# Kernel tuning notes

Measured on AMD Instinct MI355X. Metric: run time of the kernel, lower is better.

## Reference

```python
import jax, jax.numpy as jnp
import numpy as np

LATENT_DIM = 128
KQ_DIM = 32
B, N, K = 8, 16384, 16


def setup_inputs() -> dict:
    key = jax.random.key(0)
    k1, k2, k3, k4, k5, k6 = jax.random.split(key, 6)
    features = jax.random.normal(k1, (B, N, LATENT_DIM), dtype=jnp.float32)
    ks_w = jax.random.normal(k2, (KQ_DIM, LATENT_DIM), dtype=jnp.float32) * (LATENT_DIM ** -0.5)
    ks_b = jax.random.normal(k3, (KQ_DIM,), dtype=jnp.float32) * 0.01
    qs_w = jax.random.normal(k4, (KQ_DIM, LATENT_DIM), dtype=jnp.float32) * (LATENT_DIM ** -0.5)
    qs_b = jax.random.normal(k5, (KQ_DIM,), dtype=jnp.float32) * 0.01
    indices = jax.random.randint(k6, (3, B, N, K), 0, N, dtype=jnp.int64)
    return {"features": features, "ks_w": ks_w, "ks_b": ks_b,
            "qs_w": qs_w, "qs_b": qs_b, "indices": indices}


def reference(features, ks_w, ks_b, qs_w, qs_b, indices):
    # features: [B, N, latent_dim]; indices: [3, B, N, K]
    b, n, _ = features.shape
    k = indices.shape[-1]
    # Linear projections (torch Linear: x @ W^T + b)
    flatten_ks = jnp.einsum('bnl,dl->bnd', features, ks_w) + ks_b  # [B,N,D]
    flatten_qs = jnp.einsum('bnl,dl->bnd', features, qs_w) + qs_b  # [B,N,D]
    d = flatten_ks.shape[-1]
    # gather along node dim N using index channels 1 (x) and 2 (y)
    x_idx = indices[1].reshape(b, n * k)  # [B, N*K]
    y_idx = indices[2].reshape(b, n * k)
    x_features = jnp.take_along_axis(flatten_ks, x_idx[..., None], axis=1).reshape(b, n, k, d)
    y_features = jnp.take_along_axis(flatten_qs, y_idx[..., None], axis=1).reshape(b, n, k, d)
    # scaled dot-product affinity
    logits = jnp.sum(x_features * y_features, axis=-1) * (d ** -0.5)  # [B,N,K]
    return logits
```

## Files before the change

kernel.cpp:

```cpp
#include <hip/hip_runtime.h>

#define BATCH   8
#define NNODES  16384
#define KNBR    16
#define LATENT  128
#define DOUT    32
#define NROWS   (BATCH * NNODES)

typedef __attribute__((ext_vector_type(8))) short short8;
typedef __attribute__((ext_vector_type(4))) float floatx4;

__device__ __forceinline__ unsigned short f2bf(float f) {
    unsigned u = __float_as_uint(f);
    u += 0x7fff + ((u >> 16) & 1);
    return (unsigned short)(u >> 16);
}

__device__ __forceinline__ float dot2bf(unsigned a, unsigned b) {
    float alo = __uint_as_float(a << 16);
    float ahi = __uint_as_float(a & 0xffff0000u);
    float blo = __uint_as_float(b << 16);
    float bhi = __uint_as_float(b & 0xffff0000u);
    return alo * blo + ahi * bhi;
}

#define APAD 72
#define BPAD 136

__global__ __launch_bounds__(256) void proj_kernel(
    const float* __restrict__ feats,
    const float* __restrict__ kw, const float* __restrict__ kb,
    const float* __restrict__ qw, const float* __restrict__ qb,
    unsigned short* __restrict__ tkb, unsigned short* __restrict__ tqb)
{
    __shared__ unsigned short A_lds[256 * APAD];
    __shared__ unsigned short B_lds[64 * BPAD];
    __shared__ float bias_lds[64];

    const int tid  = threadIdx.x;
    const int lane = tid & 63;
    const int w    = tid >> 6;
    const long long blk_row = (long long)blockIdx.x * 256;

    {
        const float4* kw4 = (const float4*)kw;
        const float4* qw4 = (const float4*)qw;
#pragma unroll
        for (int i = 0; i < 8; ++i) {
            const int linear = i * 256 + tid;
            const int row = linear >> 5;
            const int c4  = linear & 31;
            const float4 v = (row < 32) ? kw4[row * 32 + c4] : qw4[(row - 32) * 32 + c4];
            unsigned lo = f2bf(v.x) | ((unsigned)f2bf(v.y) << 16);
            unsigned hi = f2bf(v.z) | ((unsigned)f2bf(v.w) << 16);
            *(uint2*)&B_lds[row * BPAD + c4 * 4] = make_uint2(lo, hi);
        }
        if (tid < 64) bias_lds[tid] = (tid < 32) ? kb[tid] : qb[tid - 32];
    }

    const int m = lane & 15;
    const int q = lane >> 4;

    floatx4 acc[4][4];
#pragma unroll
    for (int rt = 0; rt < 4; ++rt)
#pragma unroll
        for (int ct = 0; ct < 4; ++ct) acc[rt][ct] = (floatx4){0.f, 0.f, 0.f, 0.f};

    const float4* f4 = (const float4*)feats;
    const int s_c4   = tid & 15;
    const int s_rowg = tid >> 4;

    for (int ch = 0; ch < 2; ++ch) {
        __syncthreads();
#pragma unroll
        for (int i = 0; i < 16; ++i) {
            const int row = i * 16 + s_rowg;
            const float4 v = f4[(blk_row + row) * 32 + ch * 16 + s_c4];
            unsigned lo = f2bf(v.x) | ((unsigned)f2bf(v.y) << 16);
            unsigned hi = f2bf(v.z) | ((unsigned)f2bf(v.w) << 16);
            *(uint2*)&A_lds[row * APAD + s_c4 * 4] = make_uint2(lo, hi);
        }
        __syncthreads();

#pragma unroll
        for (int ks = 0; ks < 2; ++ks) {
            const int kk = ks * 32 + q * 8;
            const int kg = ch * 64 + kk;
            short8 bf[4];
#pragma unroll
            for (int ct = 0; ct < 4; ++ct)
                bf[ct] = *(const short8*)&B_lds[(ct * 16 + m) * BPAD + kg];
#pragma unroll
            for (int rt = 0; rt < 4; ++rt) {
                const short8 af = *(const short8*)&A_lds[(w * 64 + rt * 16 + m) * APAD + kk];
#pragma unroll
                for (int ct = 0; ct < 4; ++ct)
                    acc[rt][ct] = __builtin_amdgcn_mfma_f32_16x16x32_bf16(af, bf[ct], acc[rt][ct], 0, 0, 0);
            }
        }
    }

#pragma unroll
    for (int rt = 0; rt < 4; ++rt) {
#pragma unroll
        for (int reg = 0; reg < 4; ++reg) {
            const long long row = blk_row + w * 64 + rt * 16 + q * 4 + reg;
#pragma unroll
            for (int ct = 0; ct < 4; ++ct) {
                const float val = acc[rt][ct][reg] + bias_lds[ct * 16 + m];
                if (ct < 2) tkb[row * DOUT + ct * 16 + m]       = f2bf(val);
                else        tqb[row * DOUT + (ct - 2) * 16 + m] = f2bf(val);
            }
        }
    }
}

__global__ __launch_bounds__(256) void gather_dot_kernel(
    const unsigned short* __restrict__ tkb, const unsigned short* __restrict__ tqb,
    const int* __restrict__ idx, float* __restrict__ out)
{
    const long long NK  = (long long)NNODES * KNBR;
    const long long BNK = NK * BATCH;

    const int b   = blockIdx.x & 7;
    const int blk = blockIdx.x >> 3;
    const int grp = threadIdx.x >> 2;
    const int j   = threadIdx.x & 3;

    const uint4* tb_k = (const uint4*)(tkb + (long long)b * NNODES * DOUT);
    const uint4* tb_q = (const uint4*)(tqb + (long long)b * NNODES * DOUT);

#pragma unroll
    for (int p = 0; p < 4; ++p) {
        const long long local = (long long)blk * 256 + p * 64 + grp;
        const long long o     = (long long)b * NK + local;

        const int xi = idx[BNK + o];
        const int yi = idx[2 * BNK + o];

        const uint4 x = tb_k[(long long)xi * 4 + j];
        const uint4 y = tb_q[(long long)yi * 4 + j];
        float s = dot2bf(x.x, y.x) + dot2bf(x.y, y.y)
                + dot2bf(x.z, y.z) + dot2bf(x.w, y.w);
        s += __shfl_xor(s, 1);
        s += __shfl_xor(s, 2);
        if (j == 0) out[o] = s * 0.17677669529663687f;
    }
}

extern "C" void kernel_launch(void* const* d_in, const int* in_sizes, int n_in,
                              void* d_out, int out_size, void* d_ws, size_t ws_size,
                              hipStream_t stream)
{
    const float* feats = (const float*)d_in[0];
    const float* kw    = (const float*)d_in[1];
    const float* kb    = (const float*)d_in[2];
    const float* qw    = (const float*)d_in[3];
    const float* qb    = (const float*)d_in[4];
    const int*   idx   = (const int*)d_in[5];
    float*       out   = (float*)d_out;

    unsigned short* tkb = (unsigned short*)d_ws;
    unsigned short* tqb = tkb + (long long)NROWS * DOUT;

    proj_kernel<<<NROWS / 256, 256, 0, stream>>>(feats, kw, kb, qw, qb, tkb, tqb);
    gather_dot_kernel<<<(int)((long long)BATCH * NNODES * KNBR / 256), 256, 0, stream>>>(
        tkb, tqb, idx, out);
}
```

Measured before the change: 147.2 us.

## Load features directly to LDS with swizzle and convert to bf16 at fragment read

```diff
diff --git a/kernel.cpp b/kernel.cpp
--- a/kernel.cpp
+++ b/kernel.cpp
@@ -24,7 +24,13 @@
     return alo * blo + ahi * bhi;
 }
 
-#define APAD 72
+__device__ __forceinline__ void gload_lds16(const float* g, void* l) {
+    __builtin_amdgcn_global_load_lds(
+        (const __attribute__((address_space(1))) void*)g,
+        (__attribute__((address_space(3))) void*)l,
+        16, 0, 0);
+}
+
 #define BPAD 136
 
 __global__ __launch_bounds__(256) void proj_kernel(
@@ -33,14 +39,14 @@
     const float* __restrict__ qw, const float* __restrict__ qb,
     unsigned short* __restrict__ tkb, unsigned short* __restrict__ tqb)
 {
-    __shared__ unsigned short A_lds[256 * APAD];
+    __shared__ __align__(16) unsigned char A_raw[128 * 256];
     __shared__ unsigned short B_lds[64 * BPAD];
     __shared__ float bias_lds[64];
 
     const int tid  = threadIdx.x;
     const int lane = tid & 63;
     const int w    = tid >> 6;
-    const long long blk_row = (long long)blockIdx.x * 256;
+    const long long blk_row = (long long)blockIdx.x * 128;
 
     {
         const float4* kw4 = (const float4*)kw;
@@ -61,51 +67,55 @@
     const int m = lane & 15;
     const int q = lane >> 4;
 
-    floatx4 acc[4][4];
+    floatx4 acc[2][4];
 #pragma unroll
-    for (int rt = 0; rt < 4; ++rt)
+    for (int rt = 0; rt < 2; ++rt)
 #pragma unroll
         for (int ct = 0; ct < 4; ++ct) acc[rt][ct] = (floatx4){0.f, 0.f, 0.f, 0.f};
 
-    const float4* f4 = (const float4*)feats;
-    const int s_c4   = tid & 15;
-    const int s_rowg = tid >> 4;
+    for (int ch = 0; ch < 2; ++ch) {
+        if (ch) __syncthreads();
 
-    for (int ch = 0; ch < 2; ++ch) {
-        __syncthreads();
 #pragma unroll
-        for (int i = 0; i < 16; ++i) {
-            const int row = i * 16 + s_rowg;
-            const float4 v = f4[(blk_row + row) * 32 + ch * 16 + s_c4];
-            unsigned lo = f2bf(v.x) | ((unsigned)f2bf(v.y) << 16);
-            unsigned hi = f2bf(v.z) | ((unsigned)f2bf(v.w) << 16);
-            *(uint2*)&A_lds[row * APAD + s_c4 * 4] = make_uint2(lo, hi);
+        for (int i = 0; i < 8; ++i) {
+            const int L  = i * 4096 + tid * 16;
+            const int r  = L >> 8;
+            const int c0 = (((L & 255) ^ ((r & 7) << 4)) >> 2);
+            gload_lds16(feats + (blk_row + r) * 128 + ch * 64 + c0, A_raw + L);
         }
         __syncthreads();
 
 #pragma unroll
         for (int ks = 0; ks < 2; ++ks) {
-            const int kk = ks * 32 + q * 8;
-            const int kg = ch * 64 + kk;
+            const int kg = ch * 64 + ks * 32 + q * 8;
             short8 bf[4];
 #pragma unroll
             for (int ct = 0; ct < 4; ++ct)
                 bf[ct] = *(const short8*)&B_lds[(ct * 16 + m) * BPAD + kg];
 #pragma unroll
-            for (int rt = 0; rt < 4; ++rt) {
-                const short8 af = *(const short8*)&A_lds[(w * 64 + rt * 16 + m) * APAD + kk];
+            for (int rt = 0; rt < 2; ++rt) {
+                const int rloc = w * 32 + rt * 16 + m;
+                const int b0   = rloc * 256 + ks * 128 + q * 32;
+                const int p0   = b0 ^ ((rloc & 7) << 4);
+                const float4 a0 = *(const float4*)(A_raw + p0);
+                const float4 a1 = *(const float4*)(A_raw + (p0 ^ 16));
+                union { short8 s; unsigned u[4]; } af;
+                af.u[0] = f2bf(a0.x) | ((unsigned)f2bf(a0.y) << 16);
+                af.u[1] = f2bf(a0.z) | ((unsigned)f2bf(a0.w) << 16);
+                af.u[2] = f2bf(a1.x) | ((unsigned)f2bf(a1.y) << 16);
+                af.u[3] = f2bf(a1.z) | ((unsigned)f2bf(a1.w) << 16);
 #pragma unroll
                 for (int ct = 0; ct < 4; ++ct)
-                    acc[rt][ct] = __builtin_amdgcn_mfma_f32_16x16x32_bf16(af, bf[ct], acc[rt][ct], 0, 0, 0);
+                    acc[rt][ct] = __builtin_amdgcn_mfma_f32_16x16x32_bf16(af.s, bf[ct], acc[rt][ct], 0, 0, 0);
             }
         }
     }
 
 #pragma unroll
-    for (int rt = 0; rt < 4; ++rt) {
+    for (int rt = 0; rt < 2; ++rt) {
 #pragma unroll
         for (int reg = 0; reg < 4; ++reg) {
-            const long long row = blk_row + w * 64 + rt * 16 + q * 4 + reg;
+            const long long row = blk_row + w * 32 + rt * 16 + q * 4 + reg;
 #pragma unroll
             for (int ct = 0; ct < 4; ++ct) {
                 const float val = acc[rt][ct][reg] + bias_lds[ct * 16 + m];
@@ -136,8 +146,8 @@
         const long long local = (long long)blk * 256 + p * 64 + grp;
         const long long o     = (long long)b * NK + local;
 
-        const int xi = idx[BNK + o];
-        const int yi = idx[2 * BNK + o];
+        const int xi = __builtin_nontemporal_load(&idx[BNK + o]);
+        const int yi = __builtin_nontemporal_load(&idx[2 * BNK + o]);
 
         const uint4 x = tb_k[(long long)xi * 4 + j];
         const uint4 y = tb_q[(long long)yi * 4 + j];
@@ -145,7 +155,8 @@
                 + dot2bf(x.z, y.z) + dot2bf(x.w, y.w);
         s += __shfl_xor(s, 1);
         s += __shfl_xor(s, 2);
-        if (j == 0) out[o] = s * 0.17677669529663687f;
+        if (j == 0)
+            __builtin_nontemporal_store(s * 0.17677669529663687f, &out[o]);
     }
 }
 
@@ -164,7 +175,7 @@
     unsigned short* tkb = (unsigned short*)d_ws;
     unsigned short* tqb = tkb + (long long)NROWS * DOUT;
 
-    proj_kernel<<<NROWS / 256, 256, 0, stream>>>(feats, kw, kb, qw, qb, tkb, tqb);
+    proj_kernel<<<NROWS / 128, 256, 0, stream>>>(feats, kw, kb, qw, qb, tkb, tqb);
     gather_dot_kernel<<<(int)((long long)BATCH * NNODES * KNBR / 256), 256, 0, stream>>>(
         tkb, tqb, idx, out);
 }
```

After: 146.6 us. About the same (-0.4%).
